# Optimization experiments

Measured on AMD Instinct MI355X. Metric: run time of the kernel, lower is better.

## Reference

```python
import jax, jax.numpy as jnp
import numpy as np
import math

PHI = (1.0 + math.sqrt(5.0)) / 2.0
LN_EPS = 1e-5


def _carrier_phases(n_heads: int) -> np.ndarray:
    """Reproduce DimensionalHeadManager._allocate carrier phases."""
    base = [k * math.pi / 7.0 for k in range(7)]  # rung base phases
    n_rungs = 7
    raw = []
    remaining = n_heads
    for i in range(n_rungs):
        if i < n_rungs - 1:
            c = max(1, round(n_heads / PHI ** (i + 1)))
            c = min(c, remaining - (n_rungs - 1 - i))
            raw.append(c)
            remaining -= c
        else:
            raw.append(max(1, remaining))
    phases = []
    for rung_idx, count in enumerate(raw):
        for j in range(count):
            phases.append(base[rung_idx] + 2.0 * math.pi / max(count, 1) * j)
    return np.asarray(phases[:n_heads], dtype=np.float32)


def setup_inputs() -> dict:
    key = jax.random.key(0)
    ks = jax.random.split(key, 7)
    B, S, D, H = 2, 2048, 1024, 16
    w_scale = 0.02  # realistic init scale for Linear weights
    x = jax.random.normal(ks[0], (B, S, D), dtype=jnp.float32)
    Wq = jax.random.normal(ks[1], (D, D), dtype=jnp.float32) * w_scale
    Wk = jax.random.normal(ks[2], (D, D), dtype=jnp.float32) * w_scale
    Wv = jax.random.normal(ks[3], (D, D), dtype=jnp.float32) * w_scale
    Wo = jax.random.normal(ks[4], (D, D), dtype=jnp.float32) * w_scale
    Wp = jax.random.normal(ks[5], (D,), dtype=jnp.float32) * w_scale  # W_phase (1,D) flattened
    gamma = jnp.ones((D,), dtype=jnp.float32)
    beta = jnp.zeros((D,), dtype=jnp.float32)
    carrier = jnp.asarray(_carrier_phases(H))  # srl.carrier_freq init
    lam = jnp.float32(0.1)  # lambda_resonance init
    return {"x": x, "Wq": Wq, "Wk": Wk, "Wv": Wv, "Wo": Wo, "Wp": Wp,
            "gamma": gamma, "beta": beta, "carrier": carrier, "lam": lam}


def reference(x, Wq, Wk, Wv, Wo, Wp, gamma, beta, carrier, lam):
    B, S, D = x.shape
    H = carrier.shape[0]
    dh = D // H
    scale = 1.0 / math.sqrt(dh)

    residual = x
    # LayerNorm
    mu = jnp.mean(x, axis=-1, keepdims=True)
    var = jnp.mean((x - mu) ** 2, axis=-1, keepdims=True)
    xn = (x - mu) * jax.lax.rsqrt(var + LN_EPS) * gamma + beta

    # Q/K/V projections (torch Linear: y = x @ W.T), split into heads
    q = jnp.einsum('bsd,ed->bse', xn, Wq).reshape(B, S, H, dh)
    k = jnp.einsum('bsd,ed->bse', xn, Wk).reshape(B, S, H, dh)
    v = jnp.einsum('bsd,ed->bse', xn, Wv).reshape(B, S, H, dh)

    # scalar phase per token, per-head carrier resonance gate
    phase = jnp.einsum('bsd,d->bs', xn, Wp)                       # (B,S)
    head_T = jnp.cos((phase[..., None] - carrier) * 0.5) ** 2     # (B,S,H)

    # attention scores + resonance term R_ij = cos^2((phi_i - phi_j)/2)
    scores = jnp.einsum('bihd,bjhd->bhij', q, k) * scale          # (B,H,S,S)
    R = jnp.cos((phase[:, :, None] - phase[:, None, :]) * 0.5) ** 2  # (B,S,S)
    scores = scores + lam * R[:, None, :, :]

    attn = jax.nn.softmax(scores, axis=-1)
    out = jnp.einsum('bhij,bjhd->bihd', attn, v)                  # (B,S,H,dh)
    out = out * head_T[..., None]                                 # per-head resonance gating
    emergent_energy = jnp.sum(jnp.abs(out))
    y = residual + jnp.einsum('bse,de->bsd', out.reshape(B, S, D), Wo)
    return (y, emergent_energy)
```

## Files before the change

kernel.cpp:

```cpp
#include <hip/hip_runtime.h>
#include <hip/hip_bf16.h>

#define S_LEN 2048
#define D_MODEL 1024
#define NH 16
#define DH 64
#define M_TOK 4096
#define DK 80
#define JS 2

typedef __attribute__((ext_vector_type(8))) short bf16x8;
typedef __attribute__((ext_vector_type(4))) float f32x4;
typedef __attribute__((ext_vector_type(16))) float f32x16;

#define LOG2E 1.4426950408889634f

__device__ __forceinline__ unsigned short f2bf(float f) {
  unsigned u = __float_as_uint(f);
  u += 0x7FFF + ((u >> 16) & 1);
  return (unsigned short)(u >> 16);
}

__device__ __forceinline__ void gl16(const void* g, void* l) {
  __builtin_amdgcn_global_load_lds(
      (const __attribute__((address_space(1))) unsigned int*)g,
      (__attribute__((address_space(3))) unsigned int*)l, 16, 0, 0);
}

__device__ __forceinline__ void pl32swap(unsigned int& a, unsigned int& b) {
  asm volatile("v_permlane32_swap_b32 %0, %1" : "+v"(a), "+v"(b));
}

__global__ __launch_bounds__(256) void prep_kernel(
    const float* __restrict__ Wq, const float* __restrict__ Wk,
    const float* __restrict__ Wv, const float* __restrict__ Wo,
    unsigned short* __restrict__ wbf, float* __restrict__ energy) {
  if (blockIdx.x == 0 && threadIdx.x == 0) *energy = 0.f;
  int idx = (blockIdx.x * 256 + threadIdx.x) * 4;
  int wsel = idx >> 20;
  const float* s = (wsel == 0) ? Wq : (wsel == 1) ? Wk : (wsel == 2) ? Wv : Wo;
  int off = idx & 1048575;
  float4 v = *(const float4*)(s + off);
  ushort4 p;
  p.x = f2bf(v.x); p.y = f2bf(v.y); p.z = f2bf(v.z); p.w = f2bf(v.w);
  *(ushort4*)(wbf + idx) = p;
}

__device__ __forceinline__ float block_sum(float v, float* sm) {
#pragma unroll
  for (int o = 32; o > 0; o >>= 1) v += __shfl_xor(v, o, 64);
  int w = threadIdx.x >> 6;
  __syncthreads();
  if ((threadIdx.x & 63) == 0) sm[w] = v;
  __syncthreads();
  return sm[0] + sm[1] + sm[2] + sm[3];
}

__global__ __launch_bounds__(256) void ln_phase_kernel(
    const float* __restrict__ x, const float* __restrict__ Wp,
    const float* __restrict__ gamma, const float* __restrict__ beta,
    unsigned short* __restrict__ xn, float* __restrict__ cosP,
    float* __restrict__ sinP) {
  __shared__ float sm[4];
  int row = blockIdx.x;
  int tid = threadIdx.x;
  float4 v = ((const float4*)(x + (size_t)row * D_MODEL))[tid];
  float mu = block_sum(v.x + v.y + v.z + v.w, sm) * (1.0f / D_MODEL);
  float d0 = v.x - mu, d1 = v.y - mu, d2 = v.z - mu, d3 = v.w - mu;
  float var = block_sum(d0 * d0 + d1 * d1 + d2 * d2 + d3 * d3, sm) * (1.0f / D_MODEL);
  float rinv = rsqrtf(var + 1e-5f);
  float4 g = ((const float4*)gamma)[tid];
  float4 be = ((const float4*)beta)[tid];
  float n0 = d0 * rinv * g.x + be.x;
  float n1 = d1 * rinv * g.y + be.y;
  float n2 = d2 * rinv * g.z + be.z;
  float n3 = d3 * rinv * g.w + be.w;
  ushort4 p;
  p.x = f2bf(n0); p.y = f2bf(n1); p.z = f2bf(n2); p.w = f2bf(n3);
  ((ushort4*)(xn + (size_t)row * D_MODEL))[tid] = p;
  float4 wp = ((const float4*)Wp)[tid];
  float ph = block_sum(n0 * wp.x + n1 * wp.y + n2 * wp.z + n3 * wp.w, sm);
  if (tid == 0) {
    cosP[row] = cosf(ph);
    sinP[row] = sinf(ph);
  }
}

__global__ __launch_bounds__(256) void phase_fill_kernel(
    const float* __restrict__ cosP, const float* __restrict__ sinP,
    unsigned short* __restrict__ kk80) {
  int gid = blockIdx.x * 256 + threadIdx.x;
  int s = gid & (S_LEN - 1);
  int bh = gid >> 11;
  int b = bh >> 4;
  int tok = b * S_LEN + s;
  unsigned int w0 = (unsigned int)f2bf(cosP[tok]) | ((unsigned int)f2bf(sinP[tok]) << 16);
  *(int4*)(kk80 + (size_t)gid * DK + 64) = make_int4((int)w0, 0, 0, 0);
}

__global__ __launch_bounds__(256, 3) void qkv_gemm_kernel(
    const unsigned short* __restrict__ xn, const unsigned short* __restrict__ wbf,
    unsigned short* __restrict__ q, unsigned short* __restrict__ kk80,
    unsigned short* __restrict__ vT) {
  __shared__ __align__(16) unsigned short As[128 * 64];
  __shared__ __align__(16) unsigned short Bs[128 * 64];
  int bid = blockIdx.x;
  bool vmode = bid >= 512;
  const unsigned short* Ap;
  const unsigned short* Bp;
  int m0, n0;
  if (!vmode) {
    m0 = (bid >> 4) * 128;
    n0 = (bid & 15) * 128;
    Ap = xn; Bp = wbf;
  } else {
    int v2 = bid - 512;
    m0 = (v2 & 7) * 128;
    n0 = (v2 >> 3) * 128;
    Ap = wbf + 2 * D_MODEL * D_MODEL; Bp = xn;
  }
  int tid = threadIdx.x;
  int wave = tid >> 6, lane = tid & 63, quad = lane >> 4, l15 = lane & 15;
  int wm = (wave & 1) * 64, wn = (wave >> 1) * 64;
  f32x4 acc[4][4];
#pragma unroll
  for (int r = 0; r < 4; ++r)
#pragma unroll
    for (int c = 0; c < 4; ++c) acc[r][c] = (f32x4){0.f, 0.f, 0.f, 0.f};

  for (int k0 = 0; k0 < D_MODEL; k0 += 64) {
    __syncthreads();
#pragma unroll
    for (int t = 0; t < 4; ++t) {
      int c = t * 256 + tid;
      int r = c >> 3, p = c & 7;
      int g = p ^ (r & 7);
      gl16(&Ap[(size_t)(m0 + r) * D_MODEL + k0 + g * 8], &As[c * 8]);
      gl16(&Bp[(size_t)(n0 + r) * D_MODEL + k0 + g * 8], &Bs[c * 8]);
    }
    __syncthreads();
    bf16x8 af[4][2], bfr[4][2];
#pragma unroll
    for (int r = 0; r < 4; ++r) {
      int R = wm + r * 16 + l15;
#pragma unroll
      for (int h = 0; h < 2; ++h)
        af[r][h] = *(const bf16x8*)&As[R * 64 + ((h * 4 + quad) ^ (R & 7)) * 8];
    }
#pragma unroll
    for (int c = 0; c < 4; ++c) {
      int R = wn + c * 16 + l15;
#pragma unroll
      for (int h = 0; h < 2; ++h)
        bfr[c][h] = *(const bf16x8*)&Bs[R * 64 + ((h * 4 + quad) ^ (R & 7)) * 8];
    }
#pragma unroll
    for (int h = 0; h < 2; ++h)
#pragma unroll
      for (int r = 0; r < 4; ++r)
#pragma unroll
        for (int c = 0; c < 4; ++c)
          acc[r][c] = __builtin_amdgcn_mfma_f32_16x16x32_bf16(af[r][h], bfr[c][h], acc[r][c], 0, 0, 0);
  }
#pragma unroll
  for (int r = 0; r < 4; ++r) {
#pragma unroll
    for (int c = 0; c < 4; ++c) {
#pragma unroll
      for (int rr = 0; rr < 4; ++rr) {
        if (vmode) {
          int e = m0 + wm + r * 16 + quad * 4 + rr;
          int tok = n0 + wn + c * 16 + l15;
          int hh = e >> 6, d = e & 63;
          int bb = tok >> 11, ss = tok & (S_LEN - 1);
          vT[(((size_t)(bb * NH + hh)) * DH + d) * S_LEN + ss] = f2bf(acc[r][c][rr]);
        } else {
          int tok = m0 + wm + r * 16 + quad * 4 + rr;
          int n = n0 + wn + c * 16 + l15;
          int e = n & 1023;
          int hh = e >> 6, d = e & 63;
          int bb = tok >> 11, ss = tok & (S_LEN - 1);
          if ((n0 >> 10) == 0) {
            q[(((size_t)(bb * NH + hh)) * S_LEN + ss) * DH + d] =
                f2bf(acc[r][c][rr] * (0.125f * LOG2E));
          } else {
            kk80[(((size_t)(bb * NH + hh)) * S_LEN + ss) * DK + d] = f2bf(acc[r][c][rr]);
          }
        }
      }
    }
  }
}

__global__ __launch_bounds__(128, 4) void attn_kernel(
    const unsigned short* __restrict__ q, const unsigned short* __restrict__ kk80,
    const unsigned short* __restrict__ vT, const float* __restrict__ cosP,
    const float* __restrict__ sinP, const float* __restrict__ lamp,
    float* __restrict__ Opart, float* __restrict__ lpart) {
  __shared__ __align__(16) unsigned short Ks[64 * 72];
  __shared__ __align__(16) unsigned short Vs[512 * 8];
  int xx = blockIdx.x;
  int qt = xx & 31, js = xx >> 5;
  int h = blockIdx.y, b = blockIdx.z;
  int bh = b * NH + h;
  int tid = threadIdx.x, wave = tid >> 6, lane = tid & 63;
  int half = lane >> 5, l31 = lane & 31;

  const unsigned short* kb = kk80 + (size_t)bh * S_LEN * DK;
  const unsigned short* vb = vT + (size_t)bh * DH * S_LEN;
  int qrow = qt * 64 + wave * 32 + l31;

  bf16x8 bQ[5];
  {
    const unsigned short* qp = q + ((size_t)bh * S_LEN + qrow) * DH;
#pragma unroll
    for (int db = 0; db < 4; ++db)
      bQ[db] = *(const bf16x8*)(qp + db * 16 + half * 8);
    bf16x8 z8 = {0, 0, 0, 0, 0, 0, 0, 0};
    if (half == 0) {
      float hl2 = 0.5f * lamp[0] * LOG2E;
      z8[0] = (short)f2bf(hl2 * cosP[b * S_LEN + qrow]);
      z8[1] = (short)f2bf(hl2 * sinP[b * S_LEN + qrow]);
    }
    bQ[4] = z8;
  }

  unsigned int cc0 = tid, cc1 = tid + 128, cc2 = tid + 256, cc3 = tid + 384,
               cc4 = tid + 512;
  unsigned int kr0 = cc0 / 9u, kr1 = cc1 / 9u, kr2 = cc2 / 9u, kr3 = cc3 / 9u,
               kr4 = cc4 / 9u;
  unsigned int ko0 = kr0 * DK + (cc0 - kr0 * 9u) * 8;
  unsigned int ko1 = kr1 * DK + (cc1 - kr1 * 9u) * 8;
  unsigned int ko2 = kr2 * DK + (cc2 - kr2 * 9u) * 8;
  unsigned int ko3 = kr3 * DK + (cc3 - kr3 * 9u) * 8;
  unsigned int ko4 = kr4 * DK + (cc4 - kr4 * 9u) * 8;
  unsigned short* kl0 = (unsigned short*)Ks + cc0 * 8;
  unsigned short* kl1 = (unsigned short*)Ks + cc1 * 8;
  unsigned short* kl2 = (unsigned short*)Ks + cc2 * 8;
  unsigned short* kl3 = (unsigned short*)Ks + cc3 * 8;
  unsigned short* kl4 = (unsigned short*)Ks + cc4 * 8;
  unsigned int vr0 = cc0 >> 3, vr1 = cc1 >> 3, vr2 = cc2 >> 3, vr3 = cc3 >> 3;
  unsigned int vo0 = vr0 * S_LEN + ((cc0 & 7) ^ (vr0 & 7)) * 8;
  unsigned int vo1 = vr1 * S_LEN + ((cc1 & 7) ^ (vr1 & 7)) * 8;
  unsigned int vo2 = vr2 * S_LEN + ((cc2 & 7) ^ (vr2 & 7)) * 8;
  unsigned int vo3 = vr3 * S_LEN + ((cc3 & 7) ^ (vr3 & 7)) * 8;
  unsigned short* vl0 = (unsigned short*)Vs + cc0 * 8;
  unsigned short* vl1 = (unsigned short*)Vs + cc1 * 8;
  unsigned short* vl2 = (unsigned short*)Vs + cc2 * 8;
  unsigned short* vl3 = (unsigned short*)Vs + cc3 * 8;

  const unsigned short* kbt = kb + (size_t)(js * (S_LEN / JS)) * DK;
  const unsigned short* vbt = vb + js * (S_LEN / JS);

  f32x16 O0 = {}, O1 = {};
  float l_i = 0.f;

  for (int jt = 0; jt < S_LEN / (64 * JS); ++jt) {
    __syncthreads();
    gl16(kbt + ko0, kl0);
    gl16(kbt + ko1, kl1);
    gl16(kbt + ko2, kl2);
    gl16(kbt + ko3, kl3);
    if (tid < 64) gl16(kbt + ko4, kl4);
    gl16(vbt + vo0, vl0);
    gl16(vbt + vo1, vl1);
    gl16(vbt + vo2, vl2);
    gl16(vbt + vo3, vl3);
    kbt += 64 * DK;
    vbt += 64;
    __syncthreads();

    f32x16 Sf[2];
#pragma unroll
    for (int sj = 0; sj < 2; ++sj) {
      Sf[sj] = (f32x16){};
      int r = sj * 32 + l31;
      __builtin_amdgcn_s_setprio(1);
#pragma unroll
      for (int db = 0; db < 5; ++db) {
        int p = (db < 4) ? (db * 2 + half) : 8;
        bf16x8 aK = *(const bf16x8*)((const unsigned short*)Ks + (r * 9 + p) * 8);
        Sf[sj] = __builtin_amdgcn_mfma_f32_32x32x16_bf16(aK, bQ[db], Sf[sj], 0, 0, 0);
      }
      __builtin_amdgcn_s_setprio(0);
    }

#pragma unroll
    for (int sj = 0; sj < 2; ++sj) {
      unsigned int w[8];
#pragma unroll
      for (int rr = 0; rr < 8; ++rr) {
        float e0 = exp2f(Sf[sj][rr * 2 + 0]);
        float e1 = exp2f(Sf[sj][rr * 2 + 1]);
        l_i += e0 + e1;
        __hip_bfloat162 pk2 = __float22bfloat162_rn(float2{e0, e1});
        w[rr] = *(unsigned int*)&pk2;
      }
#pragma unroll
      for (int u = 0; u < 2; ++u) {
        unsigned int a0 = w[u * 4 + 0], a1 = w[u * 4 + 1];
        unsigned int b0 = w[u * 4 + 2], b1 = w[u * 4 + 3];
        pl32swap(a0, b0);
        pl32swap(a1, b1);
        union { unsigned int u4[4]; bf16x8 v; } cvt;
        cvt.u4[0] = a0; cvt.u4[1] = a1; cvt.u4[2] = b0; cvt.u4[3] = b1;
        int jb = sj * 2 + u;
        __builtin_amdgcn_s_setprio(1);
        {
          int rv = l31;
          int p = (jb * 2 + half) ^ (rv & 7);
          bf16x8 bV = *(const bf16x8*)((const unsigned short*)Vs + (rv * 8 + p) * 8);
          O0 = __builtin_amdgcn_mfma_f32_32x32x16_bf16(cvt.v, bV, O0, 0, 0, 0);
        }
        {
          int rv = 32 + l31;
          int p = (jb * 2 + half) ^ (rv & 7);
          bf16x8 bV = *(const bf16x8*)((const unsigned short*)Vs + (rv * 8 + p) * 8);
          O1 = __builtin_amdgcn_mfma_f32_32x32x16_bf16(cvt.v, bV, O1, 0, 0, 0);
        }
        __builtin_amdgcn_s_setprio(0);
      }
    }
  }

  l_i += __shfl_xor(l_i, 32, 64);
  size_t obase = (size_t)(js * 2 * NH + bh) * S_LEN;
#pragma unroll
  for (int reg = 0; reg < 16; ++reg) {
    int ir = (reg & 3) + 8 * (reg >> 2) + 4 * half;
    int srow = qt * 64 + wave * 32 + ir;
    Opart[(obase + srow) * DH + l31] = O0[reg];
    Opart[(obase + srow) * DH + 32 + l31] = O1[reg];
  }
  if (half == 0) lpart[obase + qt * 64 + wave * 32 + l31] = l_i;
}

__global__ __launch_bounds__(256) void combine_kernel(
    const float* __restrict__ Opart, const float* __restrict__ lpart,
    const float* __restrict__ cosP, const float* __restrict__ sinP,
    const float* __restrict__ carrier, unsigned short* __restrict__ outw,
    float* __restrict__ earray) {
  __shared__ float sm[4];
  int tok = blockIdx.x;
  int b = tok >> 11, s = tok & (S_LEN - 1);
  int t = threadIdx.x;
  int c0 = t * 4;
  int h = c0 >> 6, d0 = c0 & 63;
  int bh = b * NH + h;
  const size_t plane = (size_t)2 * NH * S_LEN;
  size_t row0 = (size_t)bh * S_LEN + s;
  float4 a0 = *(const float4*)(Opart + row0 * DH + d0);
  float4 a1 = *(const float4*)(Opart + (plane + row0) * DH + d0);
  float l = lpart[row0] + lpart[plane + row0];
  float ch = cosf(carrier[h]), sh = sinf(carrier[h]);
  float cp = cosP[tok], sp = sinP[tok];
  float gate = 0.5f + 0.5f * (cp * ch + sp * sh);
  float gl = gate / l;
  float v0 = (a0.x + a1.x) * gl, v1 = (a0.y + a1.y) * gl;
  float v2 = (a0.z + a1.z) * gl, v3 = (a0.w + a1.w) * gl;
  ushort4 p;
  p.x = f2bf(v0); p.y = f2bf(v1); p.z = f2bf(v2); p.w = f2bf(v3);
  *(ushort4*)(outw + (size_t)tok * D_MODEL + c0) = p;
  float esum = fabsf(v0) + fabsf(v1) + fabsf(v2) + fabsf(v3);
  float tot = block_sum(esum, sm);
  if (t == 0) earray[tok] = tot;
}

__global__ __launch_bounds__(256) void energy_reduce_kernel(
    const float* __restrict__ earray, float* __restrict__ energy) {
  __shared__ float sm[4];
  int t = threadIdx.x;
  float v = 0.f;
#pragma unroll
  for (int i = 0; i < 16; ++i) v += earray[t + i * 256];
  float tot = block_sum(v, sm);
  if (t == 0) *energy = tot;
}

__global__ __launch_bounds__(256) void out_gemm_kernel(
    const unsigned short* __restrict__ A, const unsigned short* __restrict__ Wo,
    const float* __restrict__ x, float* __restrict__ y) {
  __shared__ __align__(16) unsigned short As[128 * 64];
  __shared__ __align__(16) unsigned short Bs[64 * 64];
  int tid = threadIdx.x;
  int wave = tid >> 6, lane = tid & 63, quad = lane >> 4, l15 = lane & 15;
  int wm = (wave & 1) * 64, wn = (wave >> 1) * 32;
  int m0 = blockIdx.y * 128, n0 = blockIdx.x * 64;
  f32x4 acc[4][2];
#pragma unroll
  for (int r = 0; r < 4; ++r)
#pragma unroll
    for (int c = 0; c < 2; ++c) acc[r][c] = (f32x4){0.f, 0.f, 0.f, 0.f};

  for (int k0 = 0; k0 < D_MODEL; k0 += 64) {
    __syncthreads();
#pragma unroll
    for (int t = 0; t < 4; ++t) {
      int c = t * 256 + tid;
      int r = c >> 3, p = c & 7;
      int qc = p ^ (r & 7);
      gl16(&A[(size_t)(m0 + r) * D_MODEL + k0 + qc * 8], &As[c * 8]);
    }
#pragma unroll
    for (int t = 0; t < 2; ++t) {
      int c = t * 256 + tid;
      int r = c >> 3, p = c & 7;
      int qc = p ^ (r & 7);
      gl16(&Wo[(size_t)(n0 + r) * D_MODEL + k0 + qc * 8], &Bs[c * 8]);
    }
    __syncthreads();
    bf16x8 af[4][2], bfr[2][2];
#pragma unroll
    for (int r = 0; r < 4; ++r) {
      int R = wm + r * 16 + l15;
#pragma unroll
      for (int h = 0; h < 2; ++h)
        af[r][h] = *(const bf16x8*)&As[R * 64 + ((h * 4 + quad) ^ (R & 7)) * 8];
    }
#pragma unroll
    for (int c = 0; c < 2; ++c) {
      int R = wn + c * 16 + l15;
#pragma unroll
      for (int h = 0; h < 2; ++h)
        bfr[c][h] = *(const bf16x8*)&Bs[R * 64 + ((h * 4 + quad) ^ (R & 7)) * 8];
    }
#pragma unroll
    for (int h = 0; h < 2; ++h)
#pragma unroll
      for (int r = 0; r < 4; ++r)
#pragma unroll
        for (int c = 0; c < 2; ++c)
          acc[r][c] = __builtin_amdgcn_mfma_f32_16x16x32_bf16(af[r][h], bfr[c][h], acc[r][c], 0, 0, 0);
  }
#pragma unroll
  for (int r = 0; r < 4; ++r) {
#pragma unroll
    for (int c = 0; c < 2; ++c) {
      int dcol = n0 + wn + c * 16 + l15;
#pragma unroll
      for (int rr = 0; rr < 4; ++rr) {
        int tok = m0 + wm + r * 16 + quad * 4 + rr;
        size_t idx = (size_t)tok * D_MODEL + dcol;
        y[idx] = x[idx] + acc[r][c][rr];
      }
    }
  }
}

extern "C" void kernel_launch(void* const* d_in, const int* in_sizes, int n_in,
                              void* d_out, int out_size, void* d_ws, size_t ws_size,
                              hipStream_t stream) {
  const float* x = (const float*)d_in[0];
  const float* Wq = (const float*)d_in[1];
  const float* Wk = (const float*)d_in[2];
  const float* Wv = (const float*)d_in[3];
  const float* Wo = (const float*)d_in[4];
  const float* Wp = (const float*)d_in[5];
  const float* gamma = (const float*)d_in[6];
  const float* beta = (const float*)d_in[7];
  const float* carrier = (const float*)d_in[8];
  const float* lam = (const float*)d_in[9];

  char* ws = (char*)d_ws;
  const size_t MB = 1024 * 1024;
  unsigned short* wbf = (unsigned short*)(ws);
  unsigned short* xn = (unsigned short*)(ws + 8 * MB);
  unsigned short* qq = (unsigned short*)(ws + 16 * MB);
  unsigned short* kk80 = (unsigned short*)(ws + 24 * MB);
  unsigned short* vT = (unsigned short*)(ws + 34 * MB);
  float* cosP = (float*)(ws + 42 * MB);
  float* sinP = (float*)(ws + 42 * MB + 16 * 1024);
  float* Opart = (float*)(ws + 43 * MB);
  float* lpart = (float*)(ws + 75 * MB);
  float* earray = (float*)(ws + 76 * MB);
  unsigned short* outw = xn;

  float* y = (float*)d_out;
  float* energy = y + (out_size - 1);

  prep_kernel<<<4096, 256, 0, stream>>>(Wq, Wk, Wv, Wo, wbf, energy);
  ln_phase_kernel<<<M_TOK, 256, 0, stream>>>(x, Wp, gamma, beta, xn, cosP, sinP);
  phase_fill_kernel<<<256, 256, 0, stream>>>(cosP, sinP, kk80);
  qkv_gemm_kernel<<<768, 256, 0, stream>>>(xn, wbf, qq, kk80, vT);
  attn_kernel<<<dim3(32 * JS, 16, 2), 128, 0, stream>>>(qq, kk80, vT, cosP, sinP,
                                                        lam, Opart, lpart);
  combine_kernel<<<M_TOK, 256, 0, stream>>>(Opart, lpart, cosP, sinP, carrier,
                                            outw, earray);
  energy_reduce_kernel<<<1, 256, 0, stream>>>(earray, energy);
  out_gemm_kernel<<<dim3(16, 32), 256, 0, stream>>>(outw, wbf + 3 * D_MODEL * D_MODEL,
                                                    x, y);
}
```

Baseline: 226.8 us.

## Double query rows per attention wave, widen out-GEMM tile, fold small kernels away

Each attention wave now handles 64 query rows instead of 32. Every K tile and V fragment read from LDS feeds two MFMA chains, and the grid halves along the query axis. The out-projection GEMM tile grows from 128x64 to 128x128, and its first block also computes the energy reduction, so energy_reduce_kernel is removed. The phase_fill kernel is folded into the LayerNorm kernel, and the energy zeroing is dropped from prep. The changes cut kernel launches and LDS traffic per FLOP, at the cost of more registers and fewer blocks, which may hurt occupancy on the attention and out-GEMM kernels.

```diff
diff --git a/kernel.cpp b/kernel.cpp
--- a/kernel.cpp
+++ b/kernel.cpp
@@ -34,8 +34,7 @@
 __global__ __launch_bounds__(256) void prep_kernel(
     const float* __restrict__ Wq, const float* __restrict__ Wk,
     const float* __restrict__ Wv, const float* __restrict__ Wo,
-    unsigned short* __restrict__ wbf, float* __restrict__ energy) {
-  if (blockIdx.x == 0 && threadIdx.x == 0) *energy = 0.f;
+    unsigned short* __restrict__ wbf) {
   int idx = (blockIdx.x * 256 + threadIdx.x) * 4;
   int wsel = idx >> 20;
   const float* s = (wsel == 0) ? Wq : (wsel == 1) ? Wk : (wsel == 2) ? Wv : Wo;
@@ -60,7 +59,7 @@
     const float* __restrict__ x, const float* __restrict__ Wp,
     const float* __restrict__ gamma, const float* __restrict__ beta,
     unsigned short* __restrict__ xn, float* __restrict__ cosP,
-    float* __restrict__ sinP) {
+    float* __restrict__ sinP, unsigned short* __restrict__ kk80) {
   __shared__ float sm[4];
   int row = blockIdx.x;
   int tid = threadIdx.x;
@@ -84,18 +83,13 @@
     cosP[row] = cosf(ph);
     sinP[row] = sinf(ph);
   }
-}
-
-__global__ __launch_bounds__(256) void phase_fill_kernel(
-    const float* __restrict__ cosP, const float* __restrict__ sinP,
-    unsigned short* __restrict__ kk80) {
-  int gid = blockIdx.x * 256 + threadIdx.x;
-  int s = gid & (S_LEN - 1);
-  int bh = gid >> 11;
-  int b = bh >> 4;
-  int tok = b * S_LEN + s;
-  unsigned int w0 = (unsigned int)f2bf(cosP[tok]) | ((unsigned int)f2bf(sinP[tok]) << 16);
-  *(int4*)(kk80 + (size_t)gid * DK + 64) = make_int4((int)w0, 0, 0, 0);
+  if (tid < 16) {
+    float cp = cosf(ph), sp = sinf(ph);
+    unsigned int w0 = (unsigned int)f2bf(cp) | ((unsigned int)f2bf(sp) << 16);
+    int b_ = row >> 11, s_ = row & (S_LEN - 1);
+    *(int4*)(kk80 + ((size_t)((b_ * NH + tid) * S_LEN + s_)) * DK + 64) =
+        make_int4((int)w0, 0, 0, 0);
+  }
 }
 
 __global__ __launch_bounds__(256, 3) void qkv_gemm_kernel(
@@ -192,7 +186,7 @@
   }
 }
 
-__global__ __launch_bounds__(128, 4) void attn_kernel(
+__global__ __launch_bounds__(128, 2) void attn_kernel(
     const unsigned short* __restrict__ q, const unsigned short* __restrict__ kk80,
     const unsigned short* __restrict__ vT, const float* __restrict__ cosP,
     const float* __restrict__ sinP, const float* __restrict__ lamp,
@@ -200,7 +194,7 @@
   __shared__ __align__(16) unsigned short Ks[64 * 72];
   __shared__ __align__(16) unsigned short Vs[512 * 8];
   int xx = blockIdx.x;
-  int qt = xx & 31, js = xx >> 5;
+  int qt = xx & 15, js = xx >> 4;
   int h = blockIdx.y, b = blockIdx.z;
   int bh = b * NH + h;
   int tid = threadIdx.x, wave = tid >> 6, lane = tid & 63;
@@ -208,21 +202,26 @@
 
   const unsigned short* kb = kk80 + (size_t)bh * S_LEN * DK;
   const unsigned short* vb = vT + (size_t)bh * DH * S_LEN;
-  int qrow = qt * 64 + wave * 32 + l31;
-
-  bf16x8 bQ[5];
+  int i0 = qt * 128 + wave * 64;
+
+  bf16x8 bQ0[5], bQ1[5];
   {
-    const unsigned short* qp = q + ((size_t)bh * S_LEN + qrow) * DH;
-#pragma unroll
-    for (int db = 0; db < 4; ++db)
-      bQ[db] = *(const bf16x8*)(qp + db * 16 + half * 8);
-    bf16x8 z8 = {0, 0, 0, 0, 0, 0, 0, 0};
-    if (half == 0) {
-      float hl2 = 0.5f * lamp[0] * LOG2E;
-      z8[0] = (short)f2bf(hl2 * cosP[b * S_LEN + qrow]);
-      z8[1] = (short)f2bf(hl2 * sinP[b * S_LEN + qrow]);
-    }
-    bQ[4] = z8;
+    float hl2 = 0.5f * lamp[0] * LOG2E;
+#pragma unroll
+    for (int si = 0; si < 2; ++si) {
+      int qrow = i0 + si * 32 + l31;
+      const unsigned short* qp = q + ((size_t)bh * S_LEN + qrow) * DH;
+      bf16x8* dst = si ? bQ1 : bQ0;
+#pragma unroll
+      for (int db = 0; db < 4; ++db)
+        dst[db] = *(const bf16x8*)(qp + db * 16 + half * 8);
+      bf16x8 z8 = {0, 0, 0, 0, 0, 0, 0, 0};
+      if (half == 0) {
+        z8[0] = (short)f2bf(hl2 * cosP[b * S_LEN + qrow]);
+        z8[1] = (short)f2bf(hl2 * sinP[b * S_LEN + qrow]);
+      }
+      dst[4] = z8;
+    }
   }
 
   unsigned int cc0 = tid, cc1 = tid + 128, cc2 = tid + 256, cc3 = tid + 384,
@@ -252,8 +251,8 @@
   const unsigned short* kbt = kb + (size_t)(js * (S_LEN / JS)) * DK;
   const unsigned short* vbt = vb + js * (S_LEN / JS);
 
-  f32x16 O0 = {}, O1 = {};
-  float l_i = 0.f;
+  f32x16 O00 = {}, O01 = {}, O10 = {}, O11 = {};
+  float li0 = 0.f, li1 = 0.f;
 
   for (int jt = 0; jt < S_LEN / (64 * JS); ++jt) {
     __syncthreads();
@@ -270,69 +269,87 @@
     vbt += 64;
     __syncthreads();
 
-    f32x16 Sf[2];
 #pragma unroll
     for (int sj = 0; sj < 2; ++sj) {
-      Sf[sj] = (f32x16){};
+      f32x16 Sf0 = {}, Sf1 = {};
       int r = sj * 32 + l31;
       __builtin_amdgcn_s_setprio(1);
 #pragma unroll
       for (int db = 0; db < 5; ++db) {
         int p = (db < 4) ? (db * 2 + half) : 8;
         bf16x8 aK = *(const bf16x8*)((const unsigned short*)Ks + (r * 9 + p) * 8);
-        Sf[sj] = __builtin_amdgcn_mfma_f32_32x32x16_bf16(aK, bQ[db], Sf[sj], 0, 0, 0);
+        Sf0 = __builtin_amdgcn_mfma_f32_32x32x16_bf16(aK, bQ0[db], Sf0, 0, 0, 0);
+        Sf1 = __builtin_amdgcn_mfma_f32_32x32x16_bf16(aK, bQ1[db], Sf1, 0, 0, 0);
       }
       __builtin_amdgcn_s_setprio(0);
-    }
-
-#pragma unroll
-    for (int sj = 0; sj < 2; ++sj) {
-      unsigned int w[8];
-#pragma unroll
-      for (int rr = 0; rr < 8; ++rr) {
-        float e0 = exp2f(Sf[sj][rr * 2 + 0]);
-        float e1 = exp2f(Sf[sj][rr * 2 + 1]);
-        l_i += e0 + e1;
-        __hip_bfloat162 pk2 = __float22bfloat162_rn(float2{e0, e1});
-        w[rr] = *(unsigned int*)&pk2;
-      }
+
+      bf16x8 pa00, pa01, pa10, pa11;
+      auto smx = [&](const f32x16& S, float& li, bf16x8& pu0, bf16x8& pu1) {
+        unsigned int w[8];
+#pragma unroll
+        for (int rr = 0; rr < 8; ++rr) {
+          float e0 = exp2f(S[rr * 2 + 0]);
+          float e1 = exp2f(S[rr * 2 + 1]);
+          li += e0 + e1;
+          __hip_bfloat162 pk2 = __float22bfloat162_rn(float2{e0, e1});
+          w[rr] = *(unsigned int*)&pk2;
+        }
+#pragma unroll
+        for (int u = 0; u < 2; ++u) {
+          unsigned int a0 = w[u * 4 + 0], a1 = w[u * 4 + 1];
+          unsigned int b0 = w[u * 4 + 2], b1 = w[u * 4 + 3];
+          pl32swap(a0, b0);
+          pl32swap(a1, b1);
+          union { unsigned int u4[4]; bf16x8 v; } cvt;
+          cvt.u4[0] = a0; cvt.u4[1] = a1; cvt.u4[2] = b0; cvt.u4[3] = b1;
+          if (u == 0) pu0 = cvt.v; else pu1 = cvt.v;
+        }
+      };
+      smx(Sf0, li0, pa00, pa01);
+      smx(Sf1, li1, pa10, pa11);
+
 #pragma unroll
       for (int u = 0; u < 2; ++u) {
-        unsigned int a0 = w[u * 4 + 0], a1 = w[u * 4 + 1];
-        unsigned int b0 = w[u * 4 + 2], b1 = w[u * 4 + 3];
-        pl32swap(a0, b0);
-        pl32swap(a1, b1);
-        union { unsigned int u4[4]; bf16x8 v; } cvt;
-        cvt.u4[0] = a0; cvt.u4[1] = a1; cvt.u4[2] = b0; cvt.u4[3] = b1;
         int jb = sj * 2 + u;
+        bf16x8 paA = u ? pa01 : pa00;
+        bf16x8 paB = u ? pa11 : pa10;
         __builtin_amdgcn_s_setprio(1);
         {
           int rv = l31;
           int p = (jb * 2 + half) ^ (rv & 7);
           bf16x8 bV = *(const bf16x8*)((const unsigned short*)Vs + (rv * 8 + p) * 8);
-          O0 = __builtin_amdgcn_mfma_f32_32x32x16_bf16(cvt.v, bV, O0, 0, 0, 0);
+          O00 = __builtin_amdgcn_mfma_f32_32x32x16_bf16(paA, bV, O00, 0, 0, 0);
+          O10 = __builtin_amdgcn_mfma_f32_32x32x16_bf16(paB, bV, O10, 0, 0, 0);
         }
         {
           int rv = 32 + l31;
           int p = (jb * 2 + half) ^ (rv & 7);
           bf16x8 bV = *(const bf16x8*)((const unsigned short*)Vs + (rv * 8 + p) * 8);
-          O1 = __builtin_amdgcn_mfma_f32_32x32x16_bf16(cvt.v, bV, O1, 0, 0, 0);
+          O01 = __builtin_amdgcn_mfma_f32_32x32x16_bf16(paA, bV, O01, 0, 0, 0);
+          O11 = __builtin_amdgcn_mfma_f32_32x32x16_bf16(paB, bV, O11, 0, 0, 0);
         }
         __builtin_amdgcn_s_setprio(0);
       }
     }
   }
 
-  l_i += __shfl_xor(l_i, 32, 64);
+  li0 += __shfl_xor(li0, 32, 64);
+  li1 += __shfl_xor(li1, 32, 64);
   size_t obase = (size_t)(js * 2 * NH + bh) * S_LEN;
 #pragma unroll
   for (int reg = 0; reg < 16; ++reg) {
     int ir = (reg & 3) + 8 * (reg >> 2) + 4 * half;
-    int srow = qt * 64 + wave * 32 + ir;
-    Opart[(obase + srow) * DH + l31] = O0[reg];
-    Opart[(obase + srow) * DH + 32 + l31] = O1[reg];
-  }
-  if (half == 0) lpart[obase + qt * 64 + wave * 32 + l31] = l_i;
+    size_t row0 = obase + i0 + ir;
+    size_t row1 = obase + i0 + 32 + ir;
+    Opart[row0 * DH + l31] = O00[reg];
+    Opart[row0 * DH + 32 + l31] = O01[reg];
+    Opart[row1 * DH + l31] = O10[reg];
+    Opart[row1 * DH + 32 + l31] = O11[reg];
+  }
+  if (half == 0) {
+    lpart[obase + i0 + l31] = li0;
+    lpart[obase + i0 + 32 + l31] = li1;
+  }
 }
 
 __global__ __launch_bounds__(256) void combine_kernel(
@@ -366,31 +383,29 @@
   if (t == 0) earray[tok] = tot;
 }
 
-__global__ __launch_bounds__(256) void energy_reduce_kernel(
-    const float* __restrict__ earray, float* __restrict__ energy) {
+__global__ __launch_bounds__(256, 3) void out_gemm_kernel(
+    const unsigned short* __restrict__ A, const unsigned short* __restrict__ Wo,
+    const float* __restrict__ x, const float* __restrict__ earray,
+    float* __restrict__ y, float* __restrict__ energy) {
+  __shared__ __align__(16) unsigned short As[128 * 64];
+  __shared__ __align__(16) unsigned short Bs[128 * 64];
   __shared__ float sm[4];
-  int t = threadIdx.x;
-  float v = 0.f;
-#pragma unroll
-  for (int i = 0; i < 16; ++i) v += earray[t + i * 256];
-  float tot = block_sum(v, sm);
-  if (t == 0) *energy = tot;
-}
-
-__global__ __launch_bounds__(256) void out_gemm_kernel(
-    const unsigned short* __restrict__ A, const unsigned short* __restrict__ Wo,
-    const float* __restrict__ x, float* __restrict__ y) {
-  __shared__ __align__(16) unsigned short As[128 * 64];
-  __shared__ __align__(16) unsigned short Bs[64 * 64];
   int tid = threadIdx.x;
+  if (blockIdx.x == 0 && blockIdx.y == 0) {
+    float v = 0.f;
+#pragma unroll
+    for (int i = 0; i < 16; ++i) v += earray[tid + i * 256];
+    float tot = block_sum(v, sm);
+    if (tid == 0) *energy = tot;
+  }
   int wave = tid >> 6, lane = tid & 63, quad = lane >> 4, l15 = lane & 15;
-  int wm = (wave & 1) * 64, wn = (wave >> 1) * 32;
-  int m0 = blockIdx.y * 128, n0 = blockIdx.x * 64;
-  f32x4 acc[4][2];
+  int wm = (wave & 1) * 64, wn = (wave >> 1) * 64;
+  int m0 = blockIdx.y * 128, n0 = blockIdx.x * 128;
+  f32x4 acc[4][4];
 #pragma unroll
   for (int r = 0; r < 4; ++r)
 #pragma unroll
-    for (int c = 0; c < 2; ++c) acc[r][c] = (f32x4){0.f, 0.f, 0.f, 0.f};
+    for (int c = 0; c < 4; ++c) acc[r][c] = (f32x4){0.f, 0.f, 0.f, 0.f};
 
   for (int k0 = 0; k0 < D_MODEL; k0 += 64) {
     __syncthreads();
@@ -398,18 +413,12 @@
     for (int t = 0; t < 4; ++t) {
       int c = t * 256 + tid;
       int r = c >> 3, p = c & 7;
-      int qc = p ^ (r & 7);
-      gl16(&A[(size_t)(m0 + r) * D_MODEL + k0 + qc * 8], &As[c * 8]);
-    }
-#pragma unroll
-    for (int t = 0; t < 2; ++t) {
-      int c = t * 256 + tid;
-      int r = c >> 3, p = c & 7;
-      int qc = p ^ (r & 7);
-      gl16(&Wo[(size_t)(n0 + r) * D_MODEL + k0 + qc * 8], &Bs[c * 8]);
-    }
-    __syncthreads();
-    bf16x8 af[4][2], bfr[2][2];
+      int g = p ^ (r & 7);
+      gl16(&A[(size_t)(m0 + r) * D_MODEL + k0 + g * 8], &As[c * 8]);
+      gl16(&Wo[(size_t)(n0 + r) * D_MODEL + k0 + g * 8], &Bs[c * 8]);
+    }
+    __syncthreads();
+    bf16x8 af[4][2], bfr[4][2];
 #pragma unroll
     for (int r = 0; r < 4; ++r) {
       int R = wm + r * 16 + l15;
@@ -418,7 +427,7 @@
         af[r][h] = *(const bf16x8*)&As[R * 64 + ((h * 4 + quad) ^ (R & 7)) * 8];
     }
 #pragma unroll
-    for (int c = 0; c < 2; ++c) {
+    for (int c = 0; c < 4; ++c) {
       int R = wn + c * 16 + l15;
 #pragma unroll
       for (int h = 0; h < 2; ++h)
@@ -429,13 +438,13 @@
 #pragma unroll
       for (int r = 0; r < 4; ++r)
 #pragma unroll
-        for (int c = 0; c < 2; ++c)
+        for (int c = 0; c < 4; ++c)
           acc[r][c] = __builtin_amdgcn_mfma_f32_16x16x32_bf16(af[r][h], bfr[c][h], acc[r][c], 0, 0, 0);
   }
 #pragma unroll
   for (int r = 0; r < 4; ++r) {
 #pragma unroll
-    for (int c = 0; c < 2; ++c) {
+    for (int c = 0; c < 4; ++c) {
       int dcol = n0 + wn + c * 16 + l15;
 #pragma unroll
       for (int rr = 0; rr < 4; ++rr) {
@@ -478,15 +487,13 @@
   float* y = (float*)d_out;
   float* energy = y + (out_size - 1);
 
-  prep_kernel<<<4096, 256, 0, stream>>>(Wq, Wk, Wv, Wo, wbf, energy);
-  ln_phase_kernel<<<M_TOK, 256, 0, stream>>>(x, Wp, gamma, beta, xn, cosP, sinP);
-  phase_fill_kernel<<<256, 256, 0, stream>>>(cosP, sinP, kk80);
+  prep_kernel<<<4096, 256, 0, stream>>>(Wq, Wk, Wv, Wo, wbf);
+  ln_phase_kernel<<<M_TOK, 256, 0, stream>>>(x, Wp, gamma, beta, xn, cosP, sinP, kk80);
   qkv_gemm_kernel<<<768, 256, 0, stream>>>(xn, wbf, qq, kk80, vT);
-  attn_kernel<<<dim3(32 * JS, 16, 2), 128, 0, stream>>>(qq, kk80, vT, cosP, sinP,
+  attn_kernel<<<dim3(16 * JS, 16, 2), 128, 0, stream>>>(qq, kk80, vT, cosP, sinP,
                                                         lam, Opart, lpart);
   combine_kernel<<<M_TOK, 256, 0, stream>>>(Opart, lpart, cosP, sinP, carrier,
                                             outw, earray);
-  energy_reduce_kernel<<<1, 256, 0, stream>>>(earray, energy);
-  out_gemm_kernel<<<dim3(16, 32), 256, 0, stream>>>(outw, wbf + 3 * D_MODEL * D_MODEL,
-                                                    x, y);
-}
+  out_gemm_kernel<<<dim3(8, 32), 256, 0, stream>>>(outw, wbf + 3 * D_MODEL * D_MODEL,
+                                                   x, earray, y, energy);
+}
```

New measurement: 230.9 us. Within noise of the previous version (+1.8%).
